# Performance work log

Measured on AMD Instinct MI355X. Metric: run time of the kernel, lower is better.

The kernel has to match this reference:

```python
import jax, jax.numpy as jnp
import numpy as np

STRIDE, PAD, DIL, GROUPS, DG = 1, 1, 1, 1, 1
KH = KW = 3


def setup_inputs() -> dict:
    key = jax.random.key(0)
    k1, k2, k3, k4 = jax.random.split(key, 4)
    N, Cin, Cout, H, W = 8, 256, 256, 64, 64
    Ho = (H + 2 * PAD - (DIL * (KH - 1) + 1)) // STRIDE + 1
    Wo = (W + 2 * PAD - (DIL * (KW - 1) + 1)) // STRIDE + 1
    x = jax.random.normal(k1, (N, Cin, H, W), jnp.float32)
    offset = jax.random.normal(k2, (N, 2 * DG * KH * KW, Ho, Wo), jnp.float32)
    mask = jax.random.uniform(k3, (N, DG * KH * KW, Ho, Wo), jnp.float32)
    fan_in = (Cin // GROUPS) * KH * KW
    weight = jax.random.normal(k4, (Cout, Cin // GROUPS, KH, KW), jnp.float32) * np.float32(np.sqrt(2.0 / fan_in))
    bias = jnp.zeros((Cout,), jnp.float32)
    return {"x": x, "offset": offset, "mask": mask, "weight": weight, "bias": bias}


def _dcn_forward(x, offset, mask, weight, bias):
    # Modulated deformable conv v2 (DCNv2), NCHW layout.
    N, Cin, H, W = x.shape
    Cout, Cg, kh, kw = weight.shape
    K = kh * kw
    Ho, Wo = offset.shape[2], offset.shape[3]
    Cp = Cin // DG  # channels per deformable group

    # offset channels laid out as [DG, K, (dy, dx)]
    off = offset.reshape(N, DG, K, 2, Ho, Wo)
    ky = (jnp.arange(K) // kw) * DIL
    kx = (jnp.arange(K) % kw) * DIL
    base_y = (jnp.arange(Ho) * STRIDE - PAD)[None, :, None] + ky[:, None, None]  # [K,Ho,1]
    base_x = (jnp.arange(Wo) * STRIDE - PAD)[None, None, :] + kx[:, None, None]  # [K,1,Wo]
    y = base_y[None, None] + off[:, :, :, 0]   # [N,DG,K,Ho,Wo] sampling rows
    xs = base_x[None, None] + off[:, :, :, 1]  # [N,DG,K,Ho,Wo] sampling cols

    xg = x.reshape(N, DG, Cp, H * W)  # flat spatial for gathers
    y0 = jnp.floor(y)
    x0 = jnp.floor(xs)
    val = jnp.zeros((N, DG, Cp, K, Ho, Wo), x.dtype)
    # bilinear interpolation with zero padding outside the image
    for iy in (0.0, 1.0):
        for ix in (0.0, 1.0):
            yc = y0 + iy
            xc = x0 + ix
            wgt = (1.0 - jnp.abs(y - yc)) * (1.0 - jnp.abs(xs - xc))
            valid = (yc >= 0) & (yc < H) & (xc >= 0) & (xc < W)
            wgt = jnp.where(valid, wgt, 0.0)
            yci = jnp.clip(yc, 0, H - 1).astype(jnp.int32)
            xci = jnp.clip(xc, 0, W - 1).astype(jnp.int32)
            idx = (yci * W + xci).reshape(N, DG, 1, K * Ho * Wo)
            g = jnp.take_along_axis(xg, idx, axis=3).reshape(N, DG, Cp, K, Ho, Wo)
            val = val + g * wgt[:, :, None]

    # modulation mask, broadcast over channels of each deformable group
    col = val * mask.reshape(N, DG, 1, K, Ho, Wo)
    col = col.reshape(N, GROUPS, Cin // GROUPS, K, Ho, Wo)
    wr = weight.reshape(GROUPS, Cout // GROUPS, Cg, K)
    out = jnp.einsum('gock,ngckhw->ngohw', wr, col).reshape(N, Cout, Ho, Wo)
    return out + bias[None, :, None, None]


def reference(x, offset, mask, weight, bias):
    return _dcn_forward(x, offset, mask, weight, bias)
```

## Files before the change

### kernel.cpp

```cpp
#include <hip/hip_runtime.h>
#include <hip/hip_bf16.h>
#include <stdint.h>


#define XH 64
#define XW 64
#define CIN 256
#define COUT 256
#define NK 9

typedef __attribute__((ext_vector_type(8))) short short8;
typedef __attribute__((ext_vector_type(4))) float floatx4;
typedef __attribute__((ext_vector_type(2))) float floatx2;
typedef __attribute__((ext_vector_type(4))) int   intx4;

__device__ __forceinline__ short f32_to_bf16_rne(float f) {
    union { float f; uint32_t u; } v; v.f = f;
    uint32_t u = v.u;
    uint32_t r = (u + 0x7FFFu + ((u >> 16) & 1u)) >> 16;
    return (short)(uint16_t)r;
}
__device__ __forceinline__ float bf16_to_f32(short s) {
    union { uint32_t u; float f; } v;
    v.u = ((uint32_t)(uint16_t)s) << 16;
    return v.f;
}
__device__ __forceinline__ floatx2 bf16x2_to_f32x2(uint32_t u) {
    union { uint32_t u; float f; } lo, hi;
    lo.u = u << 16;
    hi.u = u & 0xFFFF0000u;
    floatx2 r; r.x = lo.f; r.y = hi.f;
    return r;
}

union U8 { short8 s; uint32_t u[4]; };

__global__ void dcn_prep(const float* __restrict__ x, const float* __restrict__ w,
                         short* __restrict__ xT, short* __restrict__ w3) {
    int b = blockIdx.x;
    int tid = threadIdx.x;
    if (b < 512) {
        int xcd = b & 7, slot = b >> 3;
        int h = xcd * 8 + (slot & 7);
        int n = slot >> 3;
        int q = tid & 15;
        int cgh = tid >> 4;
        short8* ob = (short8*)(xT + ((size_t)(n * XH + h)) * (XW * CIN));
        for (int it = 0; it < 2; ++it) {
            int cg = cgh + it * 16;
            const float* xb = x + ((size_t)(n * CIN + cg * 8)) * (XH * XW)
                                + h * XW + q * 4;
            floatx4 r[8];
#pragma unroll
            for (int j = 0; j < 8; ++j)
                r[j] = *(const floatx4*)(xb + (size_t)j * (XH * XW));
#pragma unroll
            for (int jw = 0; jw < 4; ++jw) {
                short8 pk;
#pragma unroll
                for (int j = 0; j < 8; ++j) pk[j] = f32_to_bf16_rne(r[j][jw]);
                ob[(q * 4 + jw) * 32 + cg] = pk;
            }
        }
    } else {
        int gidx = (b - 512) * 256 + tid;
        int lane = gidx & 63;
        int mt   = (gidx >> 6) & 15;
        int t    = gidx >> 10;
        int ks   = t & 7;
        int k    = t >> 3;
        int co = mt * 16 + (lane & 15);
        int c0 = ks * 32 + (lane >> 4) * 8;
        short8 pk;
#pragma unroll
        for (int j = 0; j < 8; ++j)
            pk[j] = f32_to_bf16_rne(w[(co * CIN + c0 + j) * NK + k]);
        *(short8*)&w3[(size_t)gidx * 8] = pk;
    }
}

__launch_bounds__(512, 4)
__global__ void dcn_fused5(const short* __restrict__ xT,
                           const float* __restrict__ off,
                           const float* __restrict__ msk,
                           const short* __restrict__ w3,
                           const float* __restrict__ bias,
                           float* __restrict__ out) {
    __shared__ short   colF[2][2048 * 8];
    __shared__ floatx4 pairW[576];
    __shared__ ushort4 pairO[576];

    const int bid = blockIdx.x;
    const int xcd = bid & 7, slot = bid >> 3;
    const int ho = xcd * 8 + (slot & 7);
    const int n  = slot >> 3;
    const int tid  = threadIdx.x;
    const int wave = tid >> 6;
    const int lane = tid & 63;
    const int quad = lane >> 4, cl = lane & 15;

    for (int p = tid; p < 576; p += 512) {
        int wo = p & 63, k = p >> 6;
        int obase = ((n * 18 + 2 * k) * XH + ho) * XW + wo;
        float dy = off[obase];
        float dx = off[obase + XH * XW];
        float mm = msk[((n * NK + k) * XH + ho) * XW + wo];
        float y  = (float)(ho - 1 + k / 3) + dy;
        float xs = (float)(wo - 1 + k % 3) + dx;
        float y0f = floorf(y), x0f = floorf(xs);
        float fy = y - y0f, fx = xs - x0f;
        int y0 = (int)y0f, x0 = (int)x0f;
        float vy0 = (y0 >= 0  && y0 < XH)     ? 1.f : 0.f;
        float vy1 = (y0 >= -1 && y0 < XH - 1) ? 1.f : 0.f;
        float vx0 = (x0 >= 0  && x0 < XW)     ? 1.f : 0.f;
        float vx1 = (x0 >= -1 && x0 < XW - 1) ? 1.f : 0.f;
        floatx4 wv;
        wv.x = (1.f - fy) * (1.f - fx) * mm * vy0 * vx0;
        wv.y = (1.f - fy) * fx         * mm * vy0 * vx1;
        wv.z = fy         * (1.f - fx) * mm * vy1 * vx0;
        wv.w = fy         * fx         * mm * vy1 * vx1;
        int y0c = min(max(y0, 0), XH - 1), y1c = min(max(y0 + 1, 0), XH - 1);
        int x0c = min(max(x0, 0), XW - 1), x1c = min(max(x0 + 1, 0), XW - 1);
        ushort4 ov;
        ov.x = (unsigned short)(y0c * XW + x0c);
        ov.y = (unsigned short)(y0c * XW + x1c);
        ov.z = (unsigned short)(y1c * XW + x0c);
        ov.w = (unsigned short)(y1c * XW + x1c);
        pairW[p] = wv;
        pairO[p] = ov;
    }
    __syncthreads();

    floatx4 acc[2][4];
#pragma unroll
    for (int mt = 0; mt < 2; ++mt)
#pragma unroll
        for (int nt = 0; nt < 4; ++nt)
            acc[mt][nt] = (floatx4)(0.f);

    const short8* xTv = (const short8*)(xT + (size_t)n * (XH * XW * CIN));
    const short8* w3v = (const short8*)w3;

    auto sampleTap = [&](int k, short* dst) {
        for (int it = 0; it < 4; ++it) {
            int idx = it * 512 + tid;
            int chg = idx & 31;
            int pos = idx >> 5;
            int p = k * 64 + pos;
            floatx4 wv = pairW[p];
            ushort4 ov = pairO[p];
            U8 s00, s01, s10, s11, pk;
            s00.s = xTv[(size_t)((int)ov.x * 32) + chg];
            s01.s = xTv[(size_t)((int)ov.y * 32) + chg];
            s10.s = xTv[(size_t)((int)ov.z * 32) + chg];
            s11.s = xTv[(size_t)((int)ov.w * 32) + chg];
#pragma unroll
            for (int i = 0; i < 4; ++i) {
                floatx2 v = bf16x2_to_f32x2(s00.u[i]) * wv.x
                          + bf16x2_to_f32x2(s01.u[i]) * wv.y
                          + bf16x2_to_f32x2(s10.u[i]) * wv.z
                          + bf16x2_to_f32x2(s11.u[i]) * wv.w;
                float2 ff; ff.x = v.x; ff.y = v.y;
                __hip_bfloat162 hb = __float22bfloat162_rn(ff);
                __builtin_memcpy(&pk.u[i], &hb, 4);
            }
            int g = chg * 64 + (pos ^ (chg & 7));
            *(short8*)&dst[g * 8] = pk.s;
        }
    };

    sampleTap(0, colF[0]);
    __syncthreads();

    short* cur = colF[0];
    short* nxt = colF[1];
#pragma unroll 1
    for (int k = 0; k < NK; ++k) {
        if (k < NK - 1) sampleTap(k + 1, nxt);

        const short8* cb = (const short8*)cur;
        for (int ks = 0; ks < 8; ++ks) {
            short8 afrag[2];
#pragma unroll
            for (int mt = 0; mt < 2; ++mt)
                afrag[mt] = w3v[(((k * 8 + ks) * 16) + (wave * 2 + mt)) * 64 + lane];
            short8 bfrag[4];
            int cr = ks * 4 + quad;
            int gb = cr * 64, sw = cr & 7;
#pragma unroll
            for (int nt = 0; nt < 4; ++nt)
                bfrag[nt] = cb[gb + ((nt * 16 + cl) ^ sw)];
#pragma unroll
            for (int mt = 0; mt < 2; ++mt)
#pragma unroll
                for (int nt = 0; nt < 4; ++nt)
                    acc[mt][nt] = __builtin_amdgcn_mfma_f32_16x16x32_bf16(
                        afrag[mt], bfrag[nt], acc[mt][nt], 0, 0, 0);
        }

        if (k < NK - 1) __syncthreads();
        short* t = cur; cur = nxt; nxt = t;
    }

#pragma unroll
    for (int mt = 0; mt < 2; ++mt) {
        int cobase = (wave * 2 + mt) * 16 + quad * 4;
#pragma unroll
        for (int r = 0; r < 4; ++r) {
            int co = cobase + r;
            float b = bias[co];
            float* op = out + (((size_t)n * COUT + co) * XH + ho) * XW;
#pragma unroll
            for (int nt = 0; nt < 4; ++nt)
                op[nt * 16 + cl] = acc[mt][nt][r] + b;
        }
    }
}

__global__ void dcn_wprep_v1(const float* __restrict__ w, short* __restrict__ w3) {
    int idx = blockIdx.x * 256 + threadIdx.x;
    if (idx >= 8 * 9 * 16 * 64 * 8) return;
    int j    = idx & 7;
    int lane = (idx >> 3) & 63;
    int mt   = (idx >> 9) & 15;
    int t    = idx >> 13;
    int ks   = t % 9;
    int cc   = t / 9;
    int co = mt * 16 + (lane & 15);
    int c  = cc * 32 + (lane >> 4) * 8 + j;
    w3[idx] = f32_to_bf16_rne(w[(co * CIN + c) * NK + ks]);
}

__launch_bounds__(256, 2)
__global__ void dcn_fused_v1(const float* __restrict__ x,
                             const float* __restrict__ off,
                             const float* __restrict__ msk,
                             const short* __restrict__ w3,
                             const float* __restrict__ bias,
                             float* __restrict__ out) {
    __shared__ short  colF[2304 * 8];
    __shared__ floatx4 pairW[576];
    __shared__ intx4   pairO[576];

    const int bid = blockIdx.x;
    const int n  = bid >> 6;
    const int ho = bid & 63;
    const int tid  = threadIdx.x;
    const int wave = tid >> 6;
    const int lane = tid & 63;

    for (int p = tid; p < 576; p += 256) {
        int wo = p & 63, k = p >> 6;
        int obase = ((n * 18 + 2 * k) * XH + ho) * XW + wo;
        float dy = off[obase];
        float dx = off[obase + XH * XW];
        float mm = msk[((n * NK + k) * XH + ho) * XW + wo];
        float y  = (float)(ho - 1 + k / 3) + dy;
        float xs = (float)(wo - 1 + k % 3) + dx;
        float y0f = floorf(y), x0f = floorf(xs);
        float fy = y - y0f, fx = xs - x0f;
        int y0 = (int)y0f, x0 = (int)x0f;
        float vy0 = (y0 >= 0  && y0 < XH)     ? 1.f : 0.f;
        float vy1 = (y0 >= -1 && y0 < XH - 1) ? 1.f : 0.f;
        float vx0 = (x0 >= 0  && x0 < XW)     ? 1.f : 0.f;
        float vx1 = (x0 >= -1 && x0 < XW - 1) ? 1.f : 0.f;
        floatx4 wv;
        wv.x = (1.f - fy) * (1.f - fx) * mm * vy0 * vx0;
        wv.y = (1.f - fy) * fx         * mm * vy0 * vx1;
        wv.z = fy         * (1.f - fx) * mm * vy1 * vx0;
        wv.w = fy         * fx         * mm * vy1 * vx1;
        int y0c = min(max(y0, 0), XH - 1), y1c = min(max(y0 + 1, 0), XH - 1);
        int x0c = min(max(x0, 0), XW - 1), x1c = min(max(x0 + 1, 0), XW - 1);
        intx4 ov;
        ov.x = y0c * XW + x0c; ov.y = y0c * XW + x1c;
        ov.z = y1c * XW + x0c; ov.w = y1c * XW + x1c;
        pairW[p] = wv;
        pairO[p] = ov;
    }
    __syncthreads();

    floatx4 acc[4][4];
#pragma unroll
    for (int mt = 0; mt < 4; ++mt)
#pragma unroll
        for (int nt = 0; nt < 4; ++nt)
            acc[mt][nt] = (floatx4)(0.f);

    const float* xn = x + (size_t)n * CIN * (XH * XW);
    const short8* w3v = (const short8*)w3;

    for (int cc = 0; cc < 8; ++cc) {
        __syncthreads();
        for (int it = 0; it < 9; ++it) {
            int item = it * 256 + tid;
            int pos  = item & 63;
            int r    = item >> 6;
            int k    = r >> 2;
            int csub = r & 3;
            int p = k * 64 + pos;
            floatx4 wv = pairW[p];
            intx4   ov = pairO[p];
            const float* xc = xn + (size_t)(cc * 32 + csub * 8) * (XH * XW);
            short8 pk;
#pragma unroll
            for (int i = 0; i < 8; ++i) {
                const float* xp = xc + i * (XH * XW);
                float v = wv.x * xp[ov.x] + wv.y * xp[ov.y] +
                          wv.z * xp[ov.z] + wv.w * xp[ov.w];
                pk[i] = f32_to_bf16_rne(v);
            }
            *(short8*)&colF[(((k * 4 + csub) * 64) + pos) * 8] = pk;
        }
        __syncthreads();

        const int quad = lane >> 4, cl = lane & 15;
        for (int ks = 0; ks < 9; ++ks) {
            short8 afrag[4];
#pragma unroll
            for (int mt = 0; mt < 4; ++mt) {
                int mtg = wave * 4 + mt;
                afrag[mt] = w3v[(((cc * 9 + ks) * 16 + mtg) * 64) + lane];
            }
            short8 bfrag[4];
#pragma unroll
            for (int nt = 0; nt < 4; ++nt)
                bfrag[nt] = *(const short8*)
                    &colF[(((ks * 4 + quad) * 64) + nt * 16 + cl) * 8];
#pragma unroll
            for (int mt = 0; mt < 4; ++mt)
#pragma unroll
                for (int nt = 0; nt < 4; ++nt)
                    acc[mt][nt] = __builtin_amdgcn_mfma_f32_16x16x32_bf16(
                        afrag[mt], bfrag[nt], acc[mt][nt], 0, 0, 0);
        }
    }

    const int quad = lane >> 4, cl = lane & 15;
#pragma unroll
    for (int mt = 0; mt < 4; ++mt) {
        int cobase = (wave * 4 + mt) * 16 + quad * 4;
#pragma unroll
        for (int r = 0; r < 4; ++r) {
            int co = cobase + r;
            float b = bias[co];
            float* op = out + (((size_t)n * COUT + co) * XH + ho) * XW;
#pragma unroll
            for (int nt = 0; nt < 4; ++nt)
                op[nt * 16 + cl] = acc[mt][nt][r] + b;
        }
    }
}

__global__ void dcn_naive(const float* __restrict__ x,
                          const float* __restrict__ off,
                          const float* __restrict__ msk,
                          const float* __restrict__ w,
                          const float* __restrict__ bias,
                          float* __restrict__ out) {
    int idx = blockIdx.x * 256 + threadIdx.x;
    if (idx >= 8 * COUT * XH * XW) return;
    int wo = idx & 63, ho = (idx >> 6) & 63, co = (idx >> 12) & 255, n = idx >> 20;
    float acc = bias[co];
    for (int k = 0; k < NK; ++k) {
        int obase = ((n * 18 + 2 * k) * XH + ho) * XW + wo;
        float dy = off[obase];
        float dx = off[obase + XH * XW];
        float mm = msk[((n * NK + k) * XH + ho) * XW + wo];
        float y  = (float)(ho - 1 + k / 3) + dy;
        float xs = (float)(wo - 1 + k % 3) + dx;
        float y0f = floorf(y), x0f = floorf(xs);
        float fy = y - y0f, fx = xs - x0f;
        int y0 = (int)y0f, x0 = (int)x0f;
        float vy0 = (y0 >= 0  && y0 < XH)     ? 1.f : 0.f;
        float vy1 = (y0 >= -1 && y0 < XH - 1) ? 1.f : 0.f;
        float vx0 = (x0 >= 0  && x0 < XW)     ? 1.f : 0.f;
        float vx1 = (x0 >= -1 && x0 < XW - 1) ? 1.f : 0.f;
        float w00 = (1.f - fy) * (1.f - fx) * mm * vy0 * vx0;
        float w01 = (1.f - fy) * fx         * mm * vy0 * vx1;
        float w10 = fy         * (1.f - fx) * mm * vy1 * vx0;
        float w11 = fy         * fx         * mm * vy1 * vx1;
        int y0c = min(max(y0, 0), XH - 1), y1c = min(max(y0 + 1, 0), XH - 1);
        int x0c = min(max(x0, 0), XW - 1), x1c = min(max(x0 + 1, 0), XW - 1);
        int o00 = y0c * XW + x0c, o01 = y0c * XW + x1c;
        int o10 = y1c * XW + x0c, o11 = y1c * XW + x1c;
        for (int c = 0; c < CIN; ++c) {
            const float* xp = x + ((size_t)(n * CIN + c)) * (XH * XW);
            float v = w00 * xp[o00] + w01 * xp[o01] + w10 * xp[o10] + w11 * xp[o11];
            acc += v * w[(co * CIN + c) * NK + k];
        }
    }
    out[idx] = acc;
}

extern "C" void kernel_launch(void* const* d_in, const int* in_sizes, int n_in,
                              void* d_out, int out_size, void* d_ws, size_t ws_size,
                              hipStream_t stream) {
    const float* x    = (const float*)d_in[0];
    const float* off  = (const float*)d_in[1];
    const float* msk  = (const float*)d_in[2];
    const float* w    = (const float*)d_in[3];
    const float* bias = (const float*)d_in[4];
    float* out = (float*)d_out;

    const size_t W3_BYTES = (size_t)9 * 8 * 16 * 64 * 8 * sizeof(short);
    const size_t XT_BYTES = (size_t)8 * XH * XW * CIN * sizeof(short);

    if (ws_size >= W3_BYTES + XT_BYTES) {
        short* w3 = (short*)d_ws;
        short* xT = (short*)((char*)d_ws + W3_BYTES);
        dcn_prep<<<512 + 288, 256, 0, stream>>>(x, w, xT, w3);
        dcn_fused5<<<8 * 64, 512, 0, stream>>>(xT, off, msk, w3, bias, out);
    } else if (ws_size >= W3_BYTES) {
        short* w3 = (short*)d_ws;
        dcn_wprep_v1<<<(8 * 9 * 16 * 64 * 8 + 255) / 256, 256, 0, stream>>>(w, w3);
        dcn_fused_v1<<<8 * 64, 256, 0, stream>>>(x, off, msk, w3, bias, out);
    } else {
        dcn_naive<<<(8 * COUT * XH * XW + 255) / 256, 256, 0, stream>>>(
            x, off, msk, w, bias, out);
    }
}
```

Before: 161.3 us.

## Warp-specialize fused DCN kernel into sampler and MFMA consumer waves

Splits the 8 waves of each block into 4 producer waves that do the bilinear gather of the next tap into shared memory and 4 consumer waves that run the MFMA GEMM on the current tap with 4x4 accumulator tiles. Each sampler thread now handles two adjacent 8-channel chunks. The aim is to overlap the latency-bound gathers with matrix math and to raise A-fragment reuse per wave. In exchange, consumer waves hold twice as many accumulators, which raises register pressure under the 512x4 launch bounds, and only half the waves issue each kind of work.

Result: slower. 292.2 us (+81.1%).

```diff
diff --git a/kernel.cpp b/kernel.cpp
--- a/kernel.cpp
+++ b/kernel.cpp
@@ -80,7 +80,7 @@
 }
 
 __launch_bounds__(512, 4)
-__global__ void dcn_fused5(const short* __restrict__ xT,
+__global__ void dcn_fused6(const short* __restrict__ xT,
                            const float* __restrict__ off,
                            const float* __restrict__ msk,
                            const short* __restrict__ w3,
@@ -131,88 +131,106 @@
     }
     __syncthreads();
 
-    floatx4 acc[2][4];
-#pragma unroll
-    for (int mt = 0; mt < 2; ++mt)
-#pragma unroll
-        for (int nt = 0; nt < 4; ++nt)
-            acc[mt][nt] = (floatx4)(0.f);
-
     const short8* xTv = (const short8*)(xT + (size_t)n * (XH * XW * CIN));
     const short8* w3v = (const short8*)w3;
 
     auto sampleTap = [&](int k, short* dst) {
         for (int it = 0; it < 4; ++it) {
-            int idx = it * 512 + tid;
-            int chg = idx & 31;
-            int pos = idx >> 5;
+            int idx = it * 256 + tid;
+            int cp  = idx & 15;
+            int pos = idx >> 4;
             int p = k * 64 + pos;
             floatx4 wv = pairW[p];
             ushort4 ov = pairO[p];
-            U8 s00, s01, s10, s11, pk;
-            s00.s = xTv[(size_t)((int)ov.x * 32) + chg];
-            s01.s = xTv[(size_t)((int)ov.y * 32) + chg];
-            s10.s = xTv[(size_t)((int)ov.z * 32) + chg];
-            s11.s = xTv[(size_t)((int)ov.w * 32) + chg];
+            int c0 = cp * 2;
+            const short8* q00 = xTv + ((size_t)((int)ov.x * 32 + c0));
+            const short8* q01 = xTv + ((size_t)((int)ov.y * 32 + c0));
+            const short8* q10 = xTv + ((size_t)((int)ov.z * 32 + c0));
+            const short8* q11 = xTv + ((size_t)((int)ov.w * 32 + c0));
+            U8 s00[2], s01[2], s10[2], s11[2];
+            s00[0].s = q00[0]; s00[1].s = q00[1];
+            s01[0].s = q01[0]; s01[1].s = q01[1];
+            s10[0].s = q10[0]; s10[1].s = q10[1];
+            s11[0].s = q11[0]; s11[1].s = q11[1];
+            U8 pk0, pk1;
 #pragma unroll
             for (int i = 0; i < 4; ++i) {
-                floatx2 v = bf16x2_to_f32x2(s00.u[i]) * wv.x
-                          + bf16x2_to_f32x2(s01.u[i]) * wv.y
-                          + bf16x2_to_f32x2(s10.u[i]) * wv.z
-                          + bf16x2_to_f32x2(s11.u[i]) * wv.w;
-                float2 ff; ff.x = v.x; ff.y = v.y;
-                __hip_bfloat162 hb = __float22bfloat162_rn(ff);
-                __builtin_memcpy(&pk.u[i], &hb, 4);
-            }
-            int g = chg * 64 + (pos ^ (chg & 7));
-            *(short8*)&dst[g * 8] = pk.s;
+                floatx2 v0 = bf16x2_to_f32x2(s00[0].u[i]) * wv.x
+                           + bf16x2_to_f32x2(s01[0].u[i]) * wv.y
+                           + bf16x2_to_f32x2(s10[0].u[i]) * wv.z
+                           + bf16x2_to_f32x2(s11[0].u[i]) * wv.w;
+                floatx2 v1 = bf16x2_to_f32x2(s00[1].u[i]) * wv.x
+                           + bf16x2_to_f32x2(s01[1].u[i]) * wv.y
+                           + bf16x2_to_f32x2(s10[1].u[i]) * wv.z
+                           + bf16x2_to_f32x2(s11[1].u[i]) * wv.w;
+                float2 f0; f0.x = v0.x; f0.y = v0.y;
+                float2 f1; f1.x = v1.x; f1.y = v1.y;
+                __hip_bfloat162 h0 = __float22bfloat162_rn(f0);
+                __hip_bfloat162 h1 = __float22bfloat162_rn(f1);
+                __builtin_memcpy(&pk0.u[i], &h0, 4);
+                __builtin_memcpy(&pk1.u[i], &h1, 4);
+            }
+            int g0 = c0 * 64 + (pos ^ (c0 & 7));
+            int g1 = (c0 + 1) * 64 + (pos ^ ((c0 + 1) & 7));
+            *(short8*)&dst[g0 * 8] = pk0.s;
+            *(short8*)&dst[g1 * 8] = pk1.s;
         }
     };
 
-    sampleTap(0, colF[0]);
+    floatx4 acc[4][4];
+#pragma unroll
+    for (int mt = 0; mt < 4; ++mt)
+#pragma unroll
+        for (int nt = 0; nt < 4; ++nt)
+            acc[mt][nt] = (floatx4)(0.f);
+    const int ci = wave - 4;
+
+    if (wave < 4) sampleTap(0, colF[0]);
     __syncthreads();
 
     short* cur = colF[0];
     short* nxt = colF[1];
 #pragma unroll 1
     for (int k = 0; k < NK; ++k) {
-        if (k < NK - 1) sampleTap(k + 1, nxt);
-
-        const short8* cb = (const short8*)cur;
-        for (int ks = 0; ks < 8; ++ks) {
-            short8 afrag[2];
-#pragma unroll
-            for (int mt = 0; mt < 2; ++mt)
-                afrag[mt] = w3v[(((k * 8 + ks) * 16) + (wave * 2 + mt)) * 64 + lane];
-            short8 bfrag[4];
-            int cr = ks * 4 + quad;
-            int gb = cr * 64, sw = cr & 7;
-#pragma unroll
-            for (int nt = 0; nt < 4; ++nt)
-                bfrag[nt] = cb[gb + ((nt * 16 + cl) ^ sw)];
-#pragma unroll
-            for (int mt = 0; mt < 2; ++mt)
+        if (wave < 4) {
+            if (k < NK - 1) sampleTap(k + 1, nxt);
+        } else {
+            const short8* cb = (const short8*)cur;
+            for (int ks = 0; ks < 8; ++ks) {
+                short8 bfrag[4];
+                int cr = ks * 4 + quad;
+                int gb = cr * 64, sw = cr & 7;
 #pragma unroll
                 for (int nt = 0; nt < 4; ++nt)
-                    acc[mt][nt] = __builtin_amdgcn_mfma_f32_16x16x32_bf16(
-                        afrag[mt], bfrag[nt], acc[mt][nt], 0, 0, 0);
-        }
-
-        if (k < NK - 1) __syncthreads();
+                    bfrag[nt] = cb[gb + ((nt * 16 + cl) ^ sw)];
+#pragma unroll
+                for (int mt = 0; mt < 4; ++mt) {
+                    short8 afrag =
+                        w3v[(((k * 8 + ks) * 16) + (ci * 4 + mt)) * 64 + lane];
+#pragma unroll
+                    for (int nt = 0; nt < 4; ++nt)
+                        acc[mt][nt] = __builtin_amdgcn_mfma_f32_16x16x32_bf16(
+                            afrag, bfrag[nt], acc[mt][nt], 0, 0, 0);
+                }
+            }
+        }
+        __syncthreads();
         short* t = cur; cur = nxt; nxt = t;
     }
 
-#pragma unroll
-    for (int mt = 0; mt < 2; ++mt) {
-        int cobase = (wave * 2 + mt) * 16 + quad * 4;
-#pragma unroll
-        for (int r = 0; r < 4; ++r) {
-            int co = cobase + r;
-            float b = bias[co];
-            float* op = out + (((size_t)n * COUT + co) * XH + ho) * XW;
-#pragma unroll
-            for (int nt = 0; nt < 4; ++nt)
-                op[nt * 16 + cl] = acc[mt][nt][r] + b;
+    if (wave >= 4) {
+#pragma unroll
+        for (int mt = 0; mt < 4; ++mt) {
+            int cobase = (ci * 4 + mt) * 16 + quad * 4;
+#pragma unroll
+            for (int r = 0; r < 4; ++r) {
+                int co = cobase + r;
+                float b = bias[co];
+                float* op = out + (((size_t)n * COUT + co) * XH + ho) * XW;
+#pragma unroll
+                for (int nt = 0; nt < 4; ++nt)
+                    op[nt * 16 + cl] = acc[mt][nt][r] + b;
+            }
         }
     }
 }
@@ -409,7 +427,7 @@
         short* w3 = (short*)d_ws;
         short* xT = (short*)((char*)d_ws + W3_BYTES);
         dcn_prep<<<512 + 288, 256, 0, stream>>>(x, w, xT, w3);
-        dcn_fused5<<<8 * 64, 512, 0, stream>>>(xT, off, msk, w3, bias, out);
+        dcn_fused6<<<8 * 64, 512, 0, stream>>>(xT, off, msk, w3, bias, out);
     } else if (ws_size >= W3_BYTES) {
         short* w3 = (short*)d_ws;
         dcn_wprep_v1<<<(8 * 9 * 16 * 64 * 8 + 255) / 256, 256, 0, stream>>>(w, w3);
```

## Interleave next-tap bilinear gathers with MFMA k-steps in software pipeline

Applied to the files above, without the earlier changes.

Splits the sampling of the next tap into issue (global gathers) and finish (interpolate and store to LDS) phases. These are interleaved between pairs of MFMA k-steps so gather latency is hidden behind matrix math. The tap loop is also unrolled by two with fixed double-buffer pointers. This keeps more registers live for the in-flight gathers, which could raise register pressure under the 512x4 launch bounds.

Result: slower. 171.8 us (+6.5%).

```diff
diff --git a/kernel.cpp b/kernel.cpp
--- a/kernel.cpp
+++ b/kernel.cpp
@@ -80,7 +80,7 @@
 }
 
 __launch_bounds__(512, 4)
-__global__ void dcn_fused5(const short* __restrict__ xT,
+__global__ void dcn_fused7(const short* __restrict__ xT,
                            const float* __restrict__ off,
                            const float* __restrict__ msk,
                            const short* __restrict__ w3,
@@ -141,66 +141,76 @@
     const short8* xTv = (const short8*)(xT + (size_t)n * (XH * XW * CIN));
     const short8* w3v = (const short8*)w3;
 
-    auto sampleTap = [&](int k, short* dst) {
-        for (int it = 0; it < 4; ++it) {
-            int idx = it * 512 + tid;
-            int chg = idx & 31;
-            int pos = idx >> 5;
-            int p = k * 64 + pos;
-            floatx4 wv = pairW[p];
-            ushort4 ov = pairO[p];
-            U8 s00, s01, s10, s11, pk;
-            s00.s = xTv[(size_t)((int)ov.x * 32) + chg];
-            s01.s = xTv[(size_t)((int)ov.y * 32) + chg];
-            s10.s = xTv[(size_t)((int)ov.z * 32) + chg];
-            s11.s = xTv[(size_t)((int)ov.w * 32) + chg];
-#pragma unroll
-            for (int i = 0; i < 4; ++i) {
-                floatx2 v = bf16x2_to_f32x2(s00.u[i]) * wv.x
-                          + bf16x2_to_f32x2(s01.u[i]) * wv.y
-                          + bf16x2_to_f32x2(s10.u[i]) * wv.z
-                          + bf16x2_to_f32x2(s11.u[i]) * wv.w;
-                float2 ff; ff.x = v.x; ff.y = v.y;
-                __hip_bfloat162 hb = __float22bfloat162_rn(ff);
-                __builtin_memcpy(&pk.u[i], &hb, 4);
-            }
-            int g = chg * 64 + (pos ^ (chg & 7));
-            *(short8*)&dst[g * 8] = pk.s;
-        }
+    U8 st0, st1, st2, st3;
+    int gd = 0, pp = 0;
+
+    auto ISSUE = [&](int kk, int i) {
+        int idx = i * 512 + tid;
+        int chg = idx & 31;
+        int pos = idx >> 5;
+        pp = kk * 64 + pos;
+        ushort4 ov = pairO[pp];
+        st0.s = xTv[(size_t)((int)ov.x * 32 + chg)];
+        st1.s = xTv[(size_t)((int)ov.y * 32 + chg)];
+        st2.s = xTv[(size_t)((int)ov.z * 32 + chg)];
+        st3.s = xTv[(size_t)((int)ov.w * 32 + chg)];
+        gd = chg * 64 + (pos ^ (chg & 7));
     };
-
-    sampleTap(0, colF[0]);
+    auto FINISH = [&](short* dst) {
+        floatx4 wv = pairW[pp];
+        U8 pk;
+#pragma unroll
+        for (int i = 0; i < 4; ++i) {
+            floatx2 v = bf16x2_to_f32x2(st0.u[i]) * wv.x
+                      + bf16x2_to_f32x2(st1.u[i]) * wv.y
+                      + bf16x2_to_f32x2(st2.u[i]) * wv.z
+                      + bf16x2_to_f32x2(st3.u[i]) * wv.w;
+            float2 ff; ff.x = v.x; ff.y = v.y;
+            __hip_bfloat162 hb = __float22bfloat162_rn(ff);
+            __builtin_memcpy(&pk.u[i], &hb, 4);
+        }
+        *(short8*)&dst[gd * 8] = pk.s;
+    };
+    auto KS = [&](int k, int ks, const short8* cb) {
+        short8 afrag[2];
+#pragma unroll
+        for (int mt = 0; mt < 2; ++mt)
+            afrag[mt] = w3v[(((k * 8 + ks) * 16) + (wave * 2 + mt)) * 64 + lane];
+        short8 bfrag[4];
+        int cr = ks * 4 + quad;
+        int gb = cr * 64, sw = cr & 7;
+#pragma unroll
+        for (int nt = 0; nt < 4; ++nt)
+            bfrag[nt] = cb[gb + ((nt * 16 + cl) ^ sw)];
+#pragma unroll
+        for (int mt = 0; mt < 2; ++mt)
+#pragma unroll
+            for (int nt = 0; nt < 4; ++nt)
+                acc[mt][nt] = __builtin_amdgcn_mfma_f32_16x16x32_bf16(
+                    afrag[mt], bfrag[nt], acc[mt][nt], 0, 0, 0);
+    };
+    auto tapStep = [&](int k, const short* curp, short* nxtp, bool pre) {
+        const short8* cb = (const short8*)curp;
+        if (pre) ISSUE(k + 1, 0);
+        KS(k, 0, cb); KS(k, 1, cb);
+        if (pre) { FINISH(nxtp); ISSUE(k + 1, 1); }
+        KS(k, 2, cb); KS(k, 3, cb);
+        if (pre) { FINISH(nxtp); ISSUE(k + 1, 2); }
+        KS(k, 4, cb); KS(k, 5, cb);
+        if (pre) { FINISH(nxtp); ISSUE(k + 1, 3); }
+        KS(k, 6, cb); KS(k, 7, cb);
+        if (pre) { FINISH(nxtp); __syncthreads(); }
+    };
+
+    for (int i = 0; i < 4; ++i) { ISSUE(0, i); FINISH(colF[0]); }
     __syncthreads();
 
-    short* cur = colF[0];
-    short* nxt = colF[1];
 #pragma unroll 1
-    for (int k = 0; k < NK; ++k) {
-        if (k < NK - 1) sampleTap(k + 1, nxt);
-
-        const short8* cb = (const short8*)cur;
-        for (int ks = 0; ks < 8; ++ks) {
-            short8 afrag[2];
-#pragma unroll
-            for (int mt = 0; mt < 2; ++mt)
-                afrag[mt] = w3v[(((k * 8 + ks) * 16) + (wave * 2 + mt)) * 64 + lane];
-            short8 bfrag[4];
-            int cr = ks * 4 + quad;
-            int gb = cr * 64, sw = cr & 7;
-#pragma unroll
-            for (int nt = 0; nt < 4; ++nt)
-                bfrag[nt] = cb[gb + ((nt * 16 + cl) ^ sw)];
-#pragma unroll
-            for (int mt = 0; mt < 2; ++mt)
-#pragma unroll
-                for (int nt = 0; nt < 4; ++nt)
-                    acc[mt][nt] = __builtin_amdgcn_mfma_f32_16x16x32_bf16(
-                        afrag[mt], bfrag[nt], acc[mt][nt], 0, 0, 0);
-        }
-
-        if (k < NK - 1) __syncthreads();
-        short* t = cur; cur = nxt; nxt = t;
-    }
+    for (int kp = 0; kp < 4; ++kp) {
+        tapStep(2 * kp,     colF[0], colF[1], true);
+        tapStep(2 * kp + 1, colF[1], colF[0], true);
+    }
+    tapStep(8, colF[0], colF[1], false);
 
 #pragma unroll
     for (int mt = 0; mt < 2; ++mt) {
@@ -409,7 +419,7 @@
         short* w3 = (short*)d_ws;
         short* xT = (short*)((char*)d_ws + W3_BYTES);
         dcn_prep<<<512 + 288, 256, 0, stream>>>(x, w, xT, w3);
-        dcn_fused5<<<8 * 64, 512, 0, stream>>>(xT, off, msk, w3, bias, out);
+        dcn_fused7<<<8 * 64, 512, 0, stream>>>(xT, off, msk, w3, bias, out);
     } else if (ws_size >= W3_BYTES) {
         short* w3 = (short*)d_ws;
         dcn_wprep_v1<<<(8 * 9 * 16 * 64 * 8 + 255) / 256, 256, 0, stream>>>(w, w3);
```

## Single-buffer column tile, sample two channel groups per thread, raise MFMA priority

Applied to the files above, without the earlier changes.

Drops the LDS double buffer: the next tap is now sampled after the MFMA phase behind a barrier, instead of overlapping with it. Each thread now gathers two 8-channel groups per bilinear corner (16 loads in flight), which halves the loop iterations and the shared pair-weight reads. B-fragment swizzle offsets are precomputed per lane, the ks loop is fully unrolled, and s_setprio raises wave priority around the MFMA block. The smaller LDS footprint may allow more resident blocks, but intra-block overlap of sampling and matrix math is lost and the kernel now relies on inter-block occupancy to hide latency.

Result: faster. 148.5 us (-8.0%).

```diff
diff --git a/kernel.cpp b/kernel.cpp
--- a/kernel.cpp
+++ b/kernel.cpp
@@ -80,13 +80,13 @@
 }
 
 __launch_bounds__(512, 4)
-__global__ void dcn_fused5(const short* __restrict__ xT,
+__global__ void dcn_fused8(const short* __restrict__ xT,
                            const float* __restrict__ off,
                            const float* __restrict__ msk,
                            const short* __restrict__ w3,
                            const float* __restrict__ bias,
                            float* __restrict__ out) {
-    __shared__ short   colF[2][2048 * 8];
+    __shared__ short   colF[2048 * 8];
     __shared__ floatx4 pairW[576];
     __shared__ ushort4 pairO[576];
 
@@ -141,65 +141,88 @@
     const short8* xTv = (const short8*)(xT + (size_t)n * (XH * XW * CIN));
     const short8* w3v = (const short8*)w3;
 
-    auto sampleTap = [&](int k, short* dst) {
-        for (int it = 0; it < 4; ++it) {
-            int idx = it * 512 + tid;
-            int chg = idx & 31;
-            int pos = idx >> 5;
+    int boffE[4], boffO[4];
+#pragma unroll
+    for (int nt = 0; nt < 4; ++nt) {
+        boffE[nt] = (nt * 16 + cl) ^ quad;
+        boffO[nt] = ((nt * 16 + cl) ^ quad) ^ 4;
+    }
+    const short8* cbase = (const short8*)colF;
+
+    auto sampleTap = [&](int k) {
+        for (int it = 0; it < 2; ++it) {
+            int pidx = it * 512 + tid;
+            int cp  = pidx & 15;
+            int pos = pidx >> 4;
             int p = k * 64 + pos;
+            ushort4 ov = pairO[p];
+            const short8* q00 = xTv + ((int)ov.x * 32 + cp);
+            const short8* q01 = xTv + ((int)ov.y * 32 + cp);
+            const short8* q10 = xTv + ((int)ov.z * 32 + cp);
+            const short8* q11 = xTv + ((int)ov.w * 32 + cp);
+            U8 a0, b0, c0, d0, a1, b1, c1, d1;
+            a0.s = q00[0]; a1.s = q00[16];
+            b0.s = q01[0]; b1.s = q01[16];
+            c0.s = q10[0]; c1.s = q10[16];
+            d0.s = q11[0]; d1.s = q11[16];
             floatx4 wv = pairW[p];
-            ushort4 ov = pairO[p];
-            U8 s00, s01, s10, s11, pk;
-            s00.s = xTv[(size_t)((int)ov.x * 32) + chg];
-            s01.s = xTv[(size_t)((int)ov.y * 32) + chg];
-            s10.s = xTv[(size_t)((int)ov.z * 32) + chg];
-            s11.s = xTv[(size_t)((int)ov.w * 32) + chg];
+            U8 pk0, pk1;
 #pragma unroll
             for (int i = 0; i < 4; ++i) {
-                floatx2 v = bf16x2_to_f32x2(s00.u[i]) * wv.x
-                          + bf16x2_to_f32x2(s01.u[i]) * wv.y
-                          + bf16x2_to_f32x2(s10.u[i]) * wv.z
-                          + bf16x2_to_f32x2(s11.u[i]) * wv.w;
-                float2 ff; ff.x = v.x; ff.y = v.y;
-                __hip_bfloat162 hb = __float22bfloat162_rn(ff);
-                __builtin_memcpy(&pk.u[i], &hb, 4);
+                floatx2 v0 = bf16x2_to_f32x2(a0.u[i]) * wv.x
+                           + bf16x2_to_f32x2(b0.u[i]) * wv.y
+                           + bf16x2_to_f32x2(c0.u[i]) * wv.z
+                           + bf16x2_to_f32x2(d0.u[i]) * wv.w;
+                floatx2 v1 = bf16x2_to_f32x2(a1.u[i]) * wv.x
+                           + bf16x2_to_f32x2(b1.u[i]) * wv.y
+                           + bf16x2_to_f32x2(c1.u[i]) * wv.z
+                           + bf16x2_to_f32x2(d1.u[i]) * wv.w;
+                float2 f0; f0.x = v0.x; f0.y = v0.y;
+                float2 f1; f1.x = v1.x; f1.y = v1.y;
+                __hip_bfloat162 h0 = __float22bfloat162_rn(f0);
+                __hip_bfloat162 h1 = __float22bfloat162_rn(f1);
+                __builtin_memcpy(&pk0.u[i], &h0, 4);
+                __builtin_memcpy(&pk1.u[i], &h1, 4);
             }
-            int g = chg * 64 + (pos ^ (chg & 7));
-            *(short8*)&dst[g * 8] = pk.s;
+            int sw = pos ^ (cp & 7);
+            *(short8*)&colF[(cp * 64 + sw) * 8] = pk0.s;
+            *(short8*)&colF[((cp + 16) * 64 + sw) * 8] = pk1.s;
         }
     };
 
-    sampleTap(0, colF[0]);
-    __syncthreads();
-
-    short* cur = colF[0];
-    short* nxt = colF[1];
+    sampleTap(0);
+
 #pragma unroll 1
     for (int k = 0; k < NK; ++k) {
-        if (k < NK - 1) sampleTap(k + 1, nxt);
-
-        const short8* cb = (const short8*)cur;
+        __syncthreads();
+
+        __builtin_amdgcn_s_setprio(1);
+        const short8* ap = w3v + ((k * 8 * 16) + wave * 2) * 64 + lane;
+#pragma unroll
         for (int ks = 0; ks < 8; ++ks) {
-            short8 afrag[2];
-#pragma unroll
-            for (int mt = 0; mt < 2; ++mt)
-                afrag[mt] = w3v[(((k * 8 + ks) * 16) + (wave * 2 + mt)) * 64 + lane];
+            short8 afrag0 = ap[0];
+            short8 afrag1 = ap[64];
+            const short8* cb = cbase + (ks * 256 + quad * 64);
             short8 bfrag[4];
-            int cr = ks * 4 + quad;
-            int gb = cr * 64, sw = cr & 7;
-#pragma unroll
-            for (int nt = 0; nt < 4; ++nt)
-                bfrag[nt] = cb[gb + ((nt * 16 + cl) ^ sw)];
-#pragma unroll
-            for (int mt = 0; mt < 2; ++mt)
-#pragma unroll
-                for (int nt = 0; nt < 4; ++nt)
-                    acc[mt][nt] = __builtin_amdgcn_mfma_f32_16x16x32_bf16(
-                        afrag[mt], bfrag[nt], acc[mt][nt], 0, 0, 0);
-        }
-
-        if (k < NK - 1) __syncthreads();
-        short* t = cur; cur = nxt; nxt = t;
+#pragma unroll
+            for (int nt = 0; nt < 4; ++nt)
+                bfrag[nt] = cb[(ks & 1) ? boffO[nt] : boffE[nt]];
+#pragma unroll
+            for (int nt = 0; nt < 4; ++nt)
+                acc[0][nt] = __builtin_amdgcn_mfma_f32_16x16x32_bf16(
+                    afrag0, bfrag[nt], acc[0][nt], 0, 0, 0);
+#pragma unroll
+            for (int nt = 0; nt < 4; ++nt)
+                acc[1][nt] = __builtin_amdgcn_mfma_f32_16x16x32_bf16(
+                    afrag1, bfrag[nt], acc[1][nt], 0, 0, 0);
+            ap += 16 * 64;
+        }
+        __builtin_amdgcn_s_setprio(0);
+
+        if (k < NK - 1) {
+            __syncthreads();
+            sampleTap(k + 1);
+        }
     }
 
 #pragma unroll
@@ -409,7 +432,7 @@
         short* w3 = (short*)d_ws;
         short* xT = (short*)((char*)d_ws + W3_BYTES);
         dcn_prep<<<512 + 288, 256, 0, stream>>>(x, w, xT, w3);
-        dcn_fused5<<<8 * 64, 512, 0, stream>>>(xT, off, msk, w3, bias, out);
+        dcn_fused8<<<8 * 64, 512, 0, stream>>>(xT, off, msk, w3, bias, out);
     } else if (ws_size >= W3_BYTES) {
         short* w3 = (short*)d_ws;
         dcn_wprep_v1<<<(8 * 9 * 16 * 64 * 8 + 255) / 256, 256, 0, stream>>>(w, w3);
```
